# Optimization experiments

Measured on AMD Instinct MI355X. Metric: run time of the kernel, lower is better.

The kernel has to match this reference:

```python
import jax, jax.numpy as jnp
import numpy as np

TAGSET = 256
NUM_TAGS = TAGSET + 2
START, END = TAGSET, TAGSET + 1
PAD = -1
B, S = 128, 1024


def setup_inputs() -> dict:
    key = jax.random.key(0)
    k1, k2, k3 = jax.random.split(key, 3)
    logits = jax.random.normal(k1, (B, S, TAGSET), dtype=jnp.float32)
    y = jax.random.randint(k2, (B, S), 0, TAGSET)
    # variable sequence lengths; tail padded with tag_pad_id = -1
    lengths = jax.random.randint(k3, (B,), S // 2, S + 1)
    y = jnp.where(jnp.arange(S)[None, :] < lengths[:, None], y, PAD).astype(jnp.int64)
    # transitions parameter, initialized as in CRF_Loss.__init__
    transitions = jnp.full((NUM_TAGS, NUM_TAGS), -np.log(NUM_TAGS), dtype=jnp.float32)
    transitions = transitions.at[END, :].set(-10000.0)
    transitions = transitions.at[:, START].set(-10000.0)
    return {"logits": logits, "transitions": transitions, "y": y}


def _crf_loss(logits, transitions, y):
    mask = (y != PAD).astype(logits.dtype)  # [B,S]
    s_lens = mask.sum(1)

    # ---- log Z: forward (alpha) recurrence over time via lax.scan ----
    trans_tt = transitions[:START, :START]  # [T,T]
    log_alpha = logits[:, 0] + transitions[START, :START][None, :]  # [B,T]

    def step(la, inp):
        em, m = inp  # em: [B,T], m: [B]
        # score[b,j] = logsumexp_i( la[b,i] + trans[i,j] + em[b,j] )
        score = jax.nn.logsumexp(la[:, :, None] + trans_tt[None] + em[:, None, :], axis=1)
        la = jnp.where(m[:, None] > 0, score, la)
        return la, None

    ems = jnp.swapaxes(logits[:, 1:], 0, 1)  # [S-1,B,T]
    ms = jnp.swapaxes(mask[:, 1:], 0, 1)     # [S-1,B]
    log_alpha, _ = jax.lax.scan(step, log_alpha, (ems, ms))
    log_z = jax.nn.logsumexp(log_alpha + transitions[:START, END][None, :], axis=1)  # [B]

    # ---- gold-path score log p(Y|X) numerator (vectorized over time) ----
    tags = jnp.where(y < 0, 0, y)  # clamp pads to a valid index
    llh = transitions[START, tags[:, 0]]
    llh = llh + jnp.take_along_axis(logits[:, 0], tags[:, 0:1], axis=1)[:, 0] * mask[:, 0]
    em_sc = jnp.take_along_axis(logits[:, 1:], tags[:, 1:, None], axis=2)[..., 0]  # [B,S-1]
    tr_sc = transitions[tags[:, :-1], tags[:, 1:]]                                  # [B,S-1]
    llh = llh + jnp.sum((em_sc + tr_sc) * mask[:, 1:], axis=1)
    last_idx = s_lens.astype(jnp.int32) - 1
    last_tags = jnp.take_along_axis(tags, last_idx[:, None], axis=1)[:, 0]
    llh = llh + transitions[last_tags, END]

    loss = -(llh - log_z) / s_lens
    return loss.mean()


def reference(logits, transitions, y):
    return _crf_loss(logits, transitions, y)
```

## Files before the change

### kernel.cpp

```cpp
#include <hip/hip_runtime.h>
#include <hip/hip_bf16.h>

#define B_   128
#define S_   1024
#define NT_  258
#define TG_  256
#define LN2f 0.69314718056f

typedef __attribute__((ext_vector_type(8))) short bf8_t;
typedef __attribute__((ext_vector_type(4))) float f4_t;
typedef __attribute__((ext_vector_type(4))) short s4_t;

__device__ __forceinline__ unsigned short f2bf(float f) {
  unsigned u = __float_as_uint(f);
  u += 0x7fffu + ((u >> 16) & 1u);
  return (unsigned short)(u >> 16);
}
__device__ __forceinline__ float bf2f(unsigned short s) {
  return __uint_as_float(((unsigned)s) << 16);
}

__global__ __launch_bounds__(512, 2) void crf_scan(
    const float* __restrict__ logits, const float* __restrict__ trans,
    const int* __restrict__ y, float* __restrict__ ws)
{
  __shared__ __align__(16) unsigned short aL[8192];
  __shared__ __align__(16) int   earr[16];
  __shared__ float esumL[16];
  __shared__ float refL[16];

  const int tid = threadIdx.x;
  const int w  = tid >> 6;
  const int l  = tid & 63;
  const int bq = blockIdx.x * 16;
  const int lg = l >> 4;
  const int lc = l & 15;
  const int koffe = lg * 8;

  bf8_t Bf[2][8];
#pragma unroll
  for (int ti = 0; ti < 2; ++ti) {
    const int n = 32*w + ti*16 + lc;
#pragma unroll
    for (int kk = 0; kk < 8; ++kk) {
      bf8_t bv;
#pragma unroll
      for (int e = 0; e < 8; ++e) {
        const int k = kk*32 + koffe + e;
        bv[e] = (short)f2bf(__expf(trans[k*NT_ + n]));
      }
      Bf[ti][kk] = bv;
    }
  }

  int idxA[8];
  {
    const int row = lc, sw = (row & 7) << 3;
#pragma unroll
    for (int kk = 0; kk < 8; ++kk)
      idxA[kk] = row*256 + ((kk*32 + koffe) ^ sw);
  }
  int idxW[2][4];
  int embase[2][4];
  int ybase[4];
#pragma unroll
  for (int r = 0; r < 4; ++r) {
    const int b = lg*4 + r;
    ybase[r] = (bq + b) * S_;
#pragma unroll
    for (int ti = 0; ti < 2; ++ti) {
      const int j = 32*w + ti*16 + lc;
      idxW[ti][r]   = b*256 + (j ^ ((b & 7) << 3));
      embase[ti][r] = (bq + b) * (S_*256) + j;
    }
  }

#pragma unroll
  for (int bb = 0; bb < 2; ++bb) {
    const int b = 2*w + bb;
    const float4 em0 = *(const float4*)&logits[(size_t)(bq + b) * (S_*256) + 4*l];
    const float4 ts4 = *(const float4*)&trans[TG_*NT_ + 4*l];
    const float la0 = em0.x + ts4.x, la1 = em0.y + ts4.y;
    const float la2 = em0.z + ts4.z, la3 = em0.w + ts4.w;
    const float ref = __shfl(la0, 0);
    if (l == 0) { refL[b] = ref; esumL[b] = 0.f; }
    s4_t s;
    s[0] = (short)f2bf(__expf(la0 - ref));
    s[1] = (short)f2bf(__expf(la1 - ref));
    s[2] = (short)f2bf(__expf(la2 - ref));
    s[3] = (short)f2bf(__expf(la3 - ref));
    *(s4_t*)&aL[b*256 + ((4*l) ^ ((b & 7) << 3))] = s;
  }

  float emA[2][4], emB[2][4];
  int yA[4], yB[4];
#pragma unroll
  for (int r = 0; r < 4; ++r) {
    yA[r] = y[ybase[r] + 1];
    yB[r] = y[ybase[r] + 2];
#pragma unroll
    for (int ti = 0; ti < 2; ++ti) {
      emA[ti][r] = logits[embase[ti][r] + 1*256];
      emB[ti][r] = logits[embase[ti][r] + 2*256];
    }
  }
  float esv[4] = {0.f, 0.f, 0.f, 0.f};

  __syncthreads();

#define SCAN_STEP(T_, CURE_, NXTE_, EMV_, YV_) do {                           \
  float F0_[4], F1_[4]; int m_[4];                                            \
  _Pragma("unroll") for (int r = 0; r < 4; ++r) {                             \
    F0_[r] = __expf(EMV_[0][r]); F1_[r] = __expf(EMV_[1][r]); m_[r] = YV_[r]; } \
  const int tp_ = ((T_)+2 < S_) ? ((T_)+2) : (S_-1);                          \
  _Pragma("unroll") for (int r = 0; r < 4; ++r) {                             \
    YV_[r] = y[ybase[r] + tp_];                                               \
    EMV_[0][r] = logits[embase[0][r] + tp_*256];                              \
    EMV_[1][r] = logits[embase[1][r] + tp_*256]; }                            \
  bf8_t Af_[8];                                                               \
  _Pragma("unroll") for (int kk = 0; kk < 8; ++kk)                            \
    Af_[kk] = *(const bf8_t*)&aL[(CURE_) + idxA[kk]];                         \
  f4_t c0_ = {0.f,0.f,0.f,0.f}, c1_ = {0.f,0.f,0.f,0.f};                      \
  _Pragma("unroll") for (int kk = 0; kk < 8; ++kk) {                          \
    c0_ = __builtin_amdgcn_mfma_f32_16x16x32_bf16(Af_[kk], Bf[0][kk], c0_, 0, 0, 0); \
    c1_ = __builtin_amdgcn_mfma_f32_16x16x32_bf16(Af_[kk], Bf[1][kk], c1_, 0, 0, 0); } \
  float v0_[4], v1_[4];                                                       \
  _Pragma("unroll") for (int r = 0; r < 4; ++r) {                             \
    v0_[r] = F0_[r]*c0_[r]; v1_[r] = F1_[r]*c1_[r]; }                         \
  if (((T_) & 7) == 0) {                    \
    const int4 er_ = *(const int4*)&earr[lg*4];                               \
    v0_[0] = ldexpf(v0_[0], -er_.x); v1_[0] = ldexpf(v1_[0], -er_.x);         \
    v0_[1] = ldexpf(v0_[1], -er_.y); v1_[1] = ldexpf(v1_[1], -er_.y);         \
    v0_[2] = ldexpf(v0_[2], -er_.z); v1_[2] = ldexpf(v1_[2], -er_.z);         \
    v0_[3] = ldexpf(v0_[3], -er_.w); v1_[3] = ldexpf(v1_[3], -er_.w);         \
    if (w == 0 && lc == 0) {                                                  \
      if (m_[0] >= 0) esv[0] += (float)er_.x;                                 \
      if (m_[1] >= 0) esv[1] += (float)er_.y;                                 \
      if (m_[2] >= 0) esv[2] += (float)er_.z;                                 \
      if (m_[3] >= 0) esv[3] += (float)er_.w; } }                             \
  _Pragma("unroll") for (int r = 0; r < 4; ++r) {                             \
    if (m_[r] >= 0) {                            \
      aL[(NXTE_) + idxW[0][r]] = f2bf(v0_[r]);                                \
      aL[(NXTE_) + idxW[1][r]] = f2bf(v1_[r]); } }                            \
  if (((T_) & 7) == 7 && w == 0 && lc == 0) {   \
    _Pragma("unroll") for (int r = 0; r < 4; ++r)                             \
      earr[lg*4 + r] = (int)((__float_as_uint(v0_[r]) >> 23) & 255) - 127; }  \
  asm volatile("s_waitcnt lgkmcnt(0)" ::: "memory");   \
  __builtin_amdgcn_s_barrier();                        \
  asm volatile("" ::: "memory");                       \
} while (0)

  SCAN_STEP(1, 0, 4096, emA, yA);
#pragma unroll 1
  for (int tt = 2; tt < S_; tt += 2) {
    SCAN_STEP(tt,   4096, 0, emB, yB);
    SCAN_STEP(tt+1, 0, 4096, emA, yA);
  }
#undef SCAN_STEP

  if (w == 0 && lc == 0) {
#pragma unroll
    for (int r = 0; r < 4; ++r) esumL[lg*4 + r] = esv[r];
  }
  __syncthreads();
#pragma unroll
  for (int bb = 0; bb < 2; ++bb) {
    const int b = 2*w + bb;
    const s4_t s = *(const s4_t*)&aL[4096 + b*256 + ((4*l) ^ ((b & 7) << 3))];
    float p = 0.f;
#pragma unroll
    for (int e = 0; e < 4; ++e) {
      const int k = 4*l + e;
      p += bf2f((unsigned short)s[e]) * __expf(trans[k*NT_ + 257]);
    }
#pragma unroll
    for (int o = 32; o; o >>= 1) p += __shfl_xor(p, o);
    if (l == 0)
      ws[128 + bq + b] = __logf(p) + esumL[b]*LN2f + refL[b];
  }
}

__global__ void crf_llh(const float* __restrict__ logits, const float* __restrict__ trans,
                        const int* __restrict__ y, float* __restrict__ ws)
{
  const int b = blockIdx.x, tid = threadIdx.x;
  const int yb = b * S_;
  float part = 0.f; int cnt = 0;
  for (int t = tid; t < S_; t += 256) {
    const int yt = y[yb + t];
    const bool m = (yt >= 0);
    if (m) ++cnt;
    if (t == 0) {
      const int tag0 = m ? yt : 0;
      part += trans[TG_*NT_ + tag0];
      if (m) part += logits[(size_t)yb * 256 + tag0];
    } else if (m) {
      const int yp = y[yb + t - 1];
      part += logits[((size_t)(yb + t)) * 256 + yt] + trans[yp*NT_ + yt];
    }
    if (m && (t + 1 == S_ || y[yb + t + 1] < 0))
      part += trans[yt*NT_ + 257];
  }
#pragma unroll
  for (int o = 32; o; o >>= 1) { part += __shfl_xor(part, o); cnt += __shfl_xor(cnt, o); }
  __shared__ float sp[4]; __shared__ int sc[4];
  if ((tid & 63) == 0) { sp[tid >> 6] = part; sc[tid >> 6] = cnt; }
  __syncthreads();
  if (tid == 0) {
    ws[b]       = sp[0] + sp[1] + sp[2] + sp[3];
    ws[256 + b] = (float)(sc[0] + sc[1] + sc[2] + sc[3]);
  }
}

__global__ void crf_fin(const float* __restrict__ ws, float* __restrict__ out)
{
  const int i = threadIdx.x;
  float v = -(ws[i] - ws[128 + i]) / ws[256 + i];
#pragma unroll
  for (int o = 32; o; o >>= 1) v += __shfl_xor(v, o);
  __shared__ float s2[2];
  if ((i & 63) == 0) s2[i >> 6] = v;
  __syncthreads();
  if (i == 0) out[0] = (s2[0] + s2[1]) * (1.0f / 128.0f);
}

extern "C" void kernel_launch(void* const* d_in, const int* in_sizes, int n_in,
                              void* d_out, int out_size, void* d_ws, size_t ws_size,
                              hipStream_t stream)
{
  const float* logits = (const float*)d_in[0];
  const float* trans  = (const float*)d_in[1];
  const int*   y      = (const int*)d_in[2];
  float* ws  = (float*)d_ws;
  float* out = (float*)d_out;

  hipLaunchKernelGGL(crf_llh,  dim3(128), dim3(256), 0, stream, logits, trans, y, ws);
  hipLaunchKernelGGL(crf_scan, dim3(8),   dim3(512), 0, stream, logits, trans, y, ws);
  hipLaunchKernelGGL(crf_fin,  dim3(1),   dim3(128), 0, stream, ws, out);
}
```

Before: 727.2 us.

## Halve scan workgroup to 4 waves, each computing 64 tag columns

The per-timestep scan now runs with 256 threads (4 waves) instead of 512. Each wave computes four 16-wide MFMA column tiles instead of two, so the per-step barrier synchronizes fewer waves and each wave issues more independent MFMAs. The shared-memory alpha buffer switches from an XOR swizzle to a padded row stride of 264, and bf16 conversion uses the packed v_cvt_pk_bf16_f32 instruction. The cost is more registers per wave (32 B fragments plus 16 prefetched emissions) and less wave-level parallelism per CU.

```diff
diff --git a/kernel.cpp b/kernel.cpp
--- a/kernel.cpp
+++ b/kernel.cpp
@@ -1,15 +1,15 @@
 #include <hip/hip_runtime.h>
-#include <hip/hip_bf16.h>
 
 #define B_   128
 #define S_   1024
 #define NT_  258
 #define TG_  256
 #define LN2f 0.69314718056f
+#define RSTR 264
+#define BUF  (16*RSTR)
 
 typedef __attribute__((ext_vector_type(8))) short bf8_t;
 typedef __attribute__((ext_vector_type(4))) float f4_t;
-typedef __attribute__((ext_vector_type(4))) short s4_t;
 
 __device__ __forceinline__ unsigned short f2bf(float f) {
   unsigned u = __float_as_uint(f);
@@ -19,12 +19,17 @@
 __device__ __forceinline__ float bf2f(unsigned short s) {
   return __uint_as_float(((unsigned)s) << 16);
 }
-
-__global__ __launch_bounds__(512, 2) void crf_scan(
+__device__ __forceinline__ unsigned pk_bf16(float lo, float hi) {
+  unsigned d;
+  asm("v_cvt_pk_bf16_f32 %0, %1, %2" : "=v"(d) : "v"(lo), "v"(hi));
+  return d;
+}
+
+__global__ __launch_bounds__(256, 1) void crf_scan(
     const float* __restrict__ logits, const float* __restrict__ trans,
     const int* __restrict__ y, float* __restrict__ ws)
 {
-  __shared__ __align__(16) unsigned short aL[8192];
+  __shared__ __align__(16) unsigned short aL[2*BUF];
   __shared__ __align__(16) int   earr[16];
   __shared__ float esumL[16];
   __shared__ float refL[16];
@@ -35,73 +40,65 @@
   const int bq = blockIdx.x * 16;
   const int lg = l >> 4;
   const int lc = l & 15;
-  const int koffe = lg * 8;
-
-  bf8_t Bf[2][8];
-#pragma unroll
-  for (int ti = 0; ti < 2; ++ti) {
-    const int n = 32*w + ti*16 + lc;
+
+  bf8_t Bf[4][8];
+#pragma unroll
+  for (int ti = 0; ti < 4; ++ti) {
+    const int n = 64*w + 16*ti + lc;
 #pragma unroll
     for (int kk = 0; kk < 8; ++kk) {
       bf8_t bv;
 #pragma unroll
       for (int e = 0; e < 8; ++e) {
-        const int k = kk*32 + koffe + e;
+        const int k = kk*32 + lg*8 + e;
         bv[e] = (short)f2bf(__expf(trans[k*NT_ + n]));
       }
       Bf[ti][kk] = bv;
     }
   }
 
-  int idxA[8];
+  const int idxA0 = lc*RSTR + lg*8;
+  int idxW_r[4], embase_r[4], ybase[4];
+#pragma unroll
+  for (int r = 0; r < 4; ++r) {
+    const int b = 4*lg + r;
+    idxW_r[r]   = b*RSTR + 64*w + lc;
+    embase_r[r] = (bq + b)*(S_*256) + 64*w + lc;
+    ybase[r]    = (bq + b)*S_;
+  }
+
   {
-    const int row = lc, sw = (row & 7) << 3;
-#pragma unroll
-    for (int kk = 0; kk < 8; ++kk)
-      idxA[kk] = row*256 + ((kk*32 + koffe) ^ sw);
-  }
-  int idxW[2][4];
-  int embase[2][4];
-  int ybase[4];
-#pragma unroll
-  for (int r = 0; r < 4; ++r) {
-    const int b = lg*4 + r;
-    ybase[r] = (bq + b) * S_;
-#pragma unroll
-    for (int ti = 0; ti < 2; ++ti) {
-      const int j = 32*w + ti*16 + lc;
-      idxW[ti][r]   = b*256 + (j ^ ((b & 7) << 3));
-      embase[ti][r] = (bq + b) * (S_*256) + j;
-    }
-  }
-
-#pragma unroll
-  for (int bb = 0; bb < 2; ++bb) {
-    const int b = 2*w + bb;
-    const float4 em0 = *(const float4*)&logits[(size_t)(bq + b) * (S_*256) + 4*l];
-    const float4 ts4 = *(const float4*)&trans[TG_*NT_ + 4*l];
-    const float la0 = em0.x + ts4.x, la1 = em0.y + ts4.y;
-    const float la2 = em0.z + ts4.z, la3 = em0.w + ts4.w;
-    const float ref = __shfl(la0, 0);
-    if (l == 0) { refL[b] = ref; esumL[b] = 0.f; }
-    s4_t s;
-    s[0] = (short)f2bf(__expf(la0 - ref));
-    s[1] = (short)f2bf(__expf(la1 - ref));
-    s[2] = (short)f2bf(__expf(la2 - ref));
-    s[3] = (short)f2bf(__expf(la3 - ref));
-    *(s4_t*)&aL[b*256 + ((4*l) ^ ((b & 7) << 3))] = s;
-  }
-
-  float emA[2][4], emB[2][4];
+    const int bi = tid >> 4, cb = (tid & 15) * 16;
+    if (tid < 16) {
+      refL[tid]  = logits[(size_t)(bq + tid)*(S_*256)] + trans[TG_*NT_];
+      esumL[tid] = 0.f;
+    }
+    __syncthreads();
+    const float ref = refL[bi];
+#pragma unroll
+    for (int c4 = 0; c4 < 4; ++c4) {
+      const int j = cb + 4*c4;
+      const float4 em = *(const float4*)&logits[(size_t)(bq + bi)*(S_*256) + j];
+      const float4 ts = *(const float4*)&trans[TG_*NT_ + j];
+      const unsigned d0 = pk_bf16(__expf(em.x + ts.x - ref), __expf(em.y + ts.y - ref));
+      const unsigned d1 = pk_bf16(__expf(em.z + ts.z - ref), __expf(em.w + ts.w - ref));
+      aL[bi*RSTR + j + 0] = (unsigned short)d0;
+      aL[bi*RSTR + j + 1] = (unsigned short)(d0 >> 16);
+      aL[bi*RSTR + j + 2] = (unsigned short)d1;
+      aL[bi*RSTR + j + 3] = (unsigned short)(d1 >> 16);
+    }
+  }
+
+  float emA[4][4], emB[4][4];
   int yA[4], yB[4];
 #pragma unroll
   for (int r = 0; r < 4; ++r) {
     yA[r] = y[ybase[r] + 1];
     yB[r] = y[ybase[r] + 2];
 #pragma unroll
-    for (int ti = 0; ti < 2; ++ti) {
-      emA[ti][r] = logits[embase[ti][r] + 1*256];
-      emB[ti][r] = logits[embase[ti][r] + 2*256];
+    for (int ti = 0; ti < 4; ++ti) {
+      emA[ti][r] = logits[embase_r[r] + 16*ti + 1*256];
+      emB[ti][r] = logits[embase_r[r] + 16*ti + 2*256];
     }
   }
   float esv[4] = {0.f, 0.f, 0.f, 0.f};
@@ -109,30 +106,34 @@
   __syncthreads();
 
 #define SCAN_STEP(T_, CURE_, NXTE_, EMV_, YV_) do {                           \
-  float F0_[4], F1_[4]; int m_[4];                                            \
+  bf8_t Af_[8];                                                               \
+  _Pragma("unroll") for (int kk = 0; kk < 8; ++kk)                            \
+    Af_[kk] = *(const bf8_t*)&aL[(CURE_) + idxA0 + 32*kk];                    \
+  float F_[4][4]; int m_[4];                                                  \
   _Pragma("unroll") for (int r = 0; r < 4; ++r) {                             \
-    F0_[r] = __expf(EMV_[0][r]); F1_[r] = __expf(EMV_[1][r]); m_[r] = YV_[r]; } \
+    m_[r] = YV_[r];                                                           \
+    _Pragma("unroll") for (int ti = 0; ti < 4; ++ti)                          \
+      F_[ti][r] = __expf(EMV_[ti][r]); }                                      \
   const int tp_ = ((T_)+2 < S_) ? ((T_)+2) : (S_-1);                          \
   _Pragma("unroll") for (int r = 0; r < 4; ++r) {                             \
     YV_[r] = y[ybase[r] + tp_];                                               \
-    EMV_[0][r] = logits[embase[0][r] + tp_*256];                              \
-    EMV_[1][r] = logits[embase[1][r] + tp_*256]; }                            \
-  bf8_t Af_[8];                                                               \
+    _Pragma("unroll") for (int ti = 0; ti < 4; ++ti)                          \
+      EMV_[ti][r] = logits[embase_r[r] + 16*ti + tp_*256]; }                  \
+  f4_t c_[4] = {{0,0,0,0},{0,0,0,0},{0,0,0,0},{0,0,0,0}};                     \
   _Pragma("unroll") for (int kk = 0; kk < 8; ++kk)                            \
-    Af_[kk] = *(const bf8_t*)&aL[(CURE_) + idxA[kk]];                         \
-  f4_t c0_ = {0.f,0.f,0.f,0.f}, c1_ = {0.f,0.f,0.f,0.f};                      \
-  _Pragma("unroll") for (int kk = 0; kk < 8; ++kk) {                          \
-    c0_ = __builtin_amdgcn_mfma_f32_16x16x32_bf16(Af_[kk], Bf[0][kk], c0_, 0, 0, 0); \
-    c1_ = __builtin_amdgcn_mfma_f32_16x16x32_bf16(Af_[kk], Bf[1][kk], c1_, 0, 0, 0); } \
-  float v0_[4], v1_[4];                                                       \
-  _Pragma("unroll") for (int r = 0; r < 4; ++r) {                             \
-    v0_[r] = F0_[r]*c0_[r]; v1_[r] = F1_[r]*c1_[r]; }                         \
+    _Pragma("unroll") for (int ti = 0; ti < 4; ++ti)                          \
+      c_[ti] = __builtin_amdgcn_mfma_f32_16x16x32_bf16(Af_[kk], Bf[ti][kk], c_[ti], 0, 0, 0); \
+  float v_[4][4];                                                             \
+  _Pragma("unroll") for (int ti = 0; ti < 4; ++ti)                            \
+    _Pragma("unroll") for (int r = 0; r < 4; ++r)                             \
+      v_[ti][r] = F_[ti][r]*c_[ti][r];                                        \
   if (((T_) & 7) == 0) {                    \
     const int4 er_ = *(const int4*)&earr[lg*4];                               \
-    v0_[0] = ldexpf(v0_[0], -er_.x); v1_[0] = ldexpf(v1_[0], -er_.x);         \
-    v0_[1] = ldexpf(v0_[1], -er_.y); v1_[1] = ldexpf(v1_[1], -er_.y);         \
-    v0_[2] = ldexpf(v0_[2], -er_.z); v1_[2] = ldexpf(v1_[2], -er_.z);         \
-    v0_[3] = ldexpf(v0_[3], -er_.w); v1_[3] = ldexpf(v1_[3], -er_.w);         \
+    _Pragma("unroll") for (int ti = 0; ti < 4; ++ti) {                        \
+      v_[ti][0] = ldexpf(v_[ti][0], -er_.x);                                  \
+      v_[ti][1] = ldexpf(v_[ti][1], -er_.y);                                  \
+      v_[ti][2] = ldexpf(v_[ti][2], -er_.z);                                  \
+      v_[ti][3] = ldexpf(v_[ti][3], -er_.w); }                                \
     if (w == 0 && lc == 0) {                                                  \
       if (m_[0] >= 0) esv[0] += (float)er_.x;                                 \
       if (m_[1] >= 0) esv[1] += (float)er_.y;                                 \
@@ -140,43 +141,49 @@
       if (m_[3] >= 0) esv[3] += (float)er_.w; } }                             \
   _Pragma("unroll") for (int r = 0; r < 4; ++r) {                             \
     if (m_[r] >= 0) {                            \
-      aL[(NXTE_) + idxW[0][r]] = f2bf(v0_[r]);                                \
-      aL[(NXTE_) + idxW[1][r]] = f2bf(v1_[r]); } }                            \
+      const unsigned d0_ = pk_bf16(v_[0][r], v_[1][r]);                       \
+      const unsigned d1_ = pk_bf16(v_[2][r], v_[3][r]);                       \
+      aL[(NXTE_) + idxW_r[r] +  0] = (unsigned short)d0_;                     \
+      aL[(NXTE_) + idxW_r[r] + 16] = (unsigned short)(d0_ >> 16);             \
+      aL[(NXTE_) + idxW_r[r] + 32] = (unsigned short)d1_;                     \
+      aL[(NXTE_) + idxW_r[r] + 48] = (unsigned short)(d1_ >> 16); } }         \
   if (((T_) & 7) == 7 && w == 0 && lc == 0) {   \
     _Pragma("unroll") for (int r = 0; r < 4; ++r)                             \
-      earr[lg*4 + r] = (int)((__float_as_uint(v0_[r]) >> 23) & 255) - 127; }  \
+      earr[4*lg + r] = (int)((__float_as_uint(v_[0][r]) >> 23) & 255) - 127; } \
   asm volatile("s_waitcnt lgkmcnt(0)" ::: "memory");   \
   __builtin_amdgcn_s_barrier();                        \
   asm volatile("" ::: "memory");                       \
 } while (0)
 
-  SCAN_STEP(1, 0, 4096, emA, yA);
+  SCAN_STEP(1, 0, BUF, emA, yA);
 #pragma unroll 1
   for (int tt = 2; tt < S_; tt += 2) {
-    SCAN_STEP(tt,   4096, 0, emB, yB);
-    SCAN_STEP(tt+1, 0, 4096, emA, yA);
+    SCAN_STEP(tt,   BUF, 0, emB, yB);
+    SCAN_STEP(tt+1, 0, BUF, emA, yA);
   }
 #undef SCAN_STEP
 
   if (w == 0 && lc == 0) {
 #pragma unroll
-    for (int r = 0; r < 4; ++r) esumL[lg*4 + r] = esv[r];
-  }
-  __syncthreads();
-#pragma unroll
-  for (int bb = 0; bb < 2; ++bb) {
-    const int b = 2*w + bb;
-    const s4_t s = *(const s4_t*)&aL[4096 + b*256 + ((4*l) ^ ((b & 7) << 3))];
+    for (int r = 0; r < 4; ++r) esumL[4*lg + r] = esv[r];
+  }
+  __syncthreads();
+  {
+    const int bi = tid >> 4, j0 = (tid & 15) * 16;
     float p = 0.f;
 #pragma unroll
-    for (int e = 0; e < 4; ++e) {
-      const int k = 4*l + e;
-      p += bf2f((unsigned short)s[e]) * __expf(trans[k*NT_ + 257]);
-    }
-#pragma unroll
-    for (int o = 32; o; o >>= 1) p += __shfl_xor(p, o);
-    if (l == 0)
-      ws[128 + bq + b] = __logf(p) + esumL[b]*LN2f + refL[b];
+    for (int c4 = 0; c4 < 4; ++c4) {
+      const int j = j0 + 4*c4;
+#pragma unroll
+      for (int e = 0; e < 4; ++e) {
+        const int k = j + e;
+        p += bf2f(aL[BUF + bi*RSTR + k]) * __expf(trans[k*NT_ + 257]);
+      }
+    }
+#pragma unroll
+    for (int o = 8; o; o >>= 1) p += __shfl_xor(p, o, 16);
+    if ((tid & 15) == 0)
+      ws[128 + bq + bi] = __logf(p) + esumL[bi]*LN2f + refL[bi];
   }
 }
 
@@ -235,6 +242,6 @@
   float* out = (float*)d_out;
 
   hipLaunchKernelGGL(crf_llh,  dim3(128), dim3(256), 0, stream, logits, trans, y, ws);
-  hipLaunchKernelGGL(crf_scan, dim3(8),   dim3(512), 0, stream, logits, trans, y, ws);
+  hipLaunchKernelGGL(crf_scan, dim3(8),   dim3(256), 0, stream, logits, trans, y, ws);
   hipLaunchKernelGGL(crf_fin,  dim3(1),   dim3(128), 0, stream, ws, out);
 }
```

After: 833.2 us. +14.6%, slower.
